# Kernel tuning notes

Hardware: AMD Instinct MI355X
Metric: run time of the kernel (lower is better)

## Reference

```python
import jax, jax.numpy as jnp
import numpy as np

B, T, V, E, H, D = 32, 64, 32000, 512, 1024, 1024
BOS, EOS, PAD, TAU = 1, 3, 0, 1.0


def setup_inputs() -> dict:
    key = jax.random.key(0)
    ks = jax.random.split(key, 8)
    s = lambda k, shape, sc=0.02: jax.random.normal(k, shape, jnp.float32) * sc
    return {
        'image_hidden': jax.random.normal(ks[0], (B, D), jnp.float32),
        'gumbel_u': jax.random.uniform(ks[1], (T, B, V), jnp.float32),
        'W_proj': s(ks[2], (H, D)), 'b_proj': jnp.zeros((H,), jnp.float32),
        'emb': s(ks[3], (V, E)),
        'W_ih': s(ks[4], (4 * H, E)), 'W_hh': s(ks[5], (4 * H, H)),
        'b_ih': jnp.zeros((4 * H,), jnp.float32), 'b_hh': jnp.zeros((4 * H,), jnp.float32),
        'W_hv': s(ks[6], (V, H)), 'b_hv': jnp.zeros((V,), jnp.float32),
    }


def lstm_cell(x, h, c, W_ih, W_hh, b_ih, b_hh):
    gates = x @ W_ih.T + h @ W_hh.T + (b_ih + b_hh)
    i, f, g, o = jnp.split(gates, 4, axis=-1)  # torch LSTM gate order
    c = jax.nn.sigmoid(f) * c + jax.nn.sigmoid(i) * jnp.tanh(g)
    h = jax.nn.sigmoid(o) * jnp.tanh(c)
    return h, c


def reference(image_hidden, gumbel_u, W_proj, b_proj, emb, W_ih, W_hh, b_ih, b_hh, W_hv, b_hv):
    # initial state from projected image representation
    h0 = image_hidden @ W_proj.T + b_proj            # [B, H]
    c0 = jnp.zeros_like(h0)
    x0 = jnp.broadcast_to(emb[BOS], (B, E))          # BOS embedding
    h, c = lstm_cell(x0, h0, c0, W_ih, W_hh, b_ih, b_hh)

    def step(carry, u):
        h, c = carry
        logit = h @ W_hv.T + b_hv                    # [B, V]
        g = -jnp.log(-jnp.log(u + 1e-10) + 1e-10)    # gumbel noise from uniform
        y_soft = jax.nn.softmax((logit + g) / TAU, axis=-1)
        label = jnp.argmax(y_soft, axis=-1)          # [B]
        y_hard = jax.nn.one_hot(label, V, dtype=y_soft.dtype)
        y = y_hard + y_soft - jax.lax.stop_gradient(y_soft)  # straight-through (hard=True)
        x = y @ emb                                  # soft embedding lookup [B, E]
        h, c = lstm_cell(x, h, c, W_ih, W_hh, b_ih, b_hh)
        return (h, c), (y, label)

    _, (ys, labels) = jax.lax.scan(step, (h, c), gumbel_u)
    logits = jnp.swapaxes(ys, 0, 1)                  # [B, T, V]
    labels = labels.T                                # [B, T]

    # force final token to EOS
    logits = logits.at[:, -1, :].set(jax.nn.one_hot(EOS, V, dtype=logits.dtype))
    labels = labels.at[:, -1].set(EOS)

    pad_g = jnp.cumsum((labels == EOS).astype(jnp.int32), axis=1) == 0  # True before first EOS
    message_ids = jnp.where(pad_g, labels, 0)
    pad_oh = jax.nn.one_hot(PAD, V, dtype=logits.dtype)
    message_logits = jnp.where(pad_g[:, :, None], logits, pad_oh)
    message_lengths = jnp.max(jnp.cumsum(pad_g.astype(jnp.int32), axis=1), axis=1) + 1
    return message_ids, message_logits, message_lengths
```

## Files before the change

kernel.cpp:

```cpp
#include <hip/hip_runtime.h>
#include <cstdint>
#include <cstddef>

#define NB 32
#define NT 64
#define NV 32000
#define NE 512
#define NH 1024
#define BOS_ID 1
#define EOS_ID 3
#define KC 64

__device__ __forceinline__ unsigned mono_f32(float f) {
    unsigned u = __float_as_uint(f);
    return (u & 0x80000000u) ? ~u : (u | 0x80000000u);
}

__global__ __launch_bounds__(256) void k_init(const float* __restrict__ img,
                                              const float* __restrict__ Wp,
                                              const float* __restrict__ bp,
                                              float* __restrict__ h0,
                                              float* __restrict__ c) {
    int g = blockIdx.x * 256 + threadIdx.x;
    int j = g >> 5, b = g & 31;
    const float* ir = img + (size_t)b * NH;
    const float* wr = Wp + (size_t)j * NH;
    float s = bp[j];
    for (int k = 0; k < NH; k++) s = fmaf(ir[k], wr[k], s);
    h0[b * NH + j] = s;
    c[b * NH + j]  = 0.0f;
}

__global__ __launch_bounds__(512) void k_logit(const float* __restrict__ h,
                                               const float* __restrict__ Whv,
                                               const float* __restrict__ bhv,
                                               const float* __restrict__ gu,
                                               int s,
                                               unsigned long long* __restrict__ slot) {
    __shared__ float wsh[2][KC][132];
    __shared__ float hs[2][KC][34];
    const int tid = threadIdx.x;
    const int v0  = blockIdx.x * 128;
    const int vq  = tid & 31;
    const int bq  = tid >> 5;
    const int wq  = tid & 15;
    const int wv  = tid >> 4;

    float4 wr[4];
    float4 hr;
    float acc[2][4];
#pragma unroll
    for (int bi = 0; bi < 2; bi++)
#pragma unroll
        for (int j = 0; j < 4; j++) acc[bi][j] = 0.f;

    auto load_chunk = [&](int kc) {
#pragma unroll
        for (int i = 0; i < 4; i++) {
            int vv = i * 32 + wv;
            wr[i] = *(const float4*)&Whv[(size_t)(v0 + vv) * NH + kc + wq * 4];
        }
        hr = *(const float4*)&h[wv * NH + kc + wq * 4];
    };
    auto store_chunk = [&](int p) {
#pragma unroll
        for (int i = 0; i < 4; i++) {
            int vv = i * 32 + wv;
            wsh[p][wq * 4 + 0][vv] = wr[i].x;
            wsh[p][wq * 4 + 1][vv] = wr[i].y;
            wsh[p][wq * 4 + 2][vv] = wr[i].z;
            wsh[p][wq * 4 + 3][vv] = wr[i].w;
        }
        hs[p][wq * 4 + 0][wv] = hr.x;
        hs[p][wq * 4 + 1][wv] = hr.y;
        hs[p][wq * 4 + 2][wv] = hr.z;
        hs[p][wq * 4 + 3][wv] = hr.w;
    };

    load_chunk(0);
    store_chunk(0);
    load_chunk(KC);

    const int NCH = NH / KC;
    for (int c = 0; c < NCH; c++) {
        __syncthreads();
        const int p = c & 1;
#pragma unroll 16
        for (int kk = 0; kk < KC; kk++) {
            float4 wv4 = *(const float4*)&wsh[p][kk][vq * 4];
            float2 hv2 = *(const float2*)&hs[p][kk][bq * 2];
            acc[0][0] = fmaf(hv2.x, wv4.x, acc[0][0]);
            acc[0][1] = fmaf(hv2.x, wv4.y, acc[0][1]);
            acc[0][2] = fmaf(hv2.x, wv4.z, acc[0][2]);
            acc[0][3] = fmaf(hv2.x, wv4.w, acc[0][3]);
            acc[1][0] = fmaf(hv2.y, wv4.x, acc[1][0]);
            acc[1][1] = fmaf(hv2.y, wv4.y, acc[1][1]);
            acc[1][2] = fmaf(hv2.y, wv4.z, acc[1][2]);
            acc[1][3] = fmaf(hv2.y, wv4.w, acc[1][3]);
        }
        if (c + 1 < NCH) {
            store_chunk(1 - p);
            if (c + 2 < NCH) load_chunk((c + 2) * KC);
        }
    }

    const float4 bv4 = *(const float4*)&bhv[v0 + vq * 4];
    float bvv[4] = {bv4.x, bv4.y, bv4.z, bv4.w};
    unsigned long long key[2];
#pragma unroll
    for (int bi = 0; bi < 2; bi++) {
        int b = bq * 2 + bi;
        const float4 u4 = *(const float4*)&gu[((size_t)s * NB + b) * NV + v0 + vq * 4];
        float uvv[4] = {u4.x, u4.y, u4.z, u4.w};
        float best = -3.4e38f;
        int bidx = v0 + vq * 4;
#pragma unroll
        for (int j = 0; j < 4; j++) {
            float g  = -logf(-logf(uvv[j] + 1e-10f) + 1e-10f);
            float sc = acc[bi][j] + bvv[j] + g;
            if (sc > best) { best = sc; bidx = v0 + vq * 4 + j; }
        }
        key[bi] = ((unsigned long long)mono_f32(best) << 32) | (unsigned)(~(unsigned)bidx);
    }
#pragma unroll
    for (int m = 1; m < 32; m <<= 1) {
#pragma unroll
        for (int bi = 0; bi < 2; bi++) {
            unsigned long long o =
                (unsigned long long)__shfl_xor((long long)key[bi], m, 32);
            if (o > key[bi]) key[bi] = o;
        }
    }
    if (vq == 0) {
#pragma unroll
        for (int bi = 0; bi < 2; bi++)
            atomicMax(&slot[(s & 1) * 32 + bq * 2 + bi], key[bi]);
    }
}

__global__ __launch_bounds__(256) void k_lstm(const float* __restrict__ h,
                                              float* __restrict__ hn,
                                              float* __restrict__ cbuf,
                                              const float* __restrict__ emb,
                                              const float* __restrict__ Wih,
                                              const float* __restrict__ Whh,
                                              const float* __restrict__ bih,
                                              const float* __restrict__ bhh,
                                              unsigned long long* __restrict__ slot,
                                              int* __restrict__ hist,
                                              int s, int skip) {
    __shared__ float Wt[512][20];
    __shared__ float xh[32][517];
    __shared__ int labels[32];
    const int tid = threadIdx.x, blk = blockIdx.x;
    const int b8 = tid >> 3, ks = tid & 7;

    if (s < 0) {
        if (tid < 32) labels[tid] = BOS_ID;
    } else {
        if (tid < 32) labels[tid] = (int)(~(unsigned)slot[(s & 1) * 32 + tid]);
    }
    if (tid >= 32 && tid < 64)
        slot[((s + 1) & 1) * 32 + (tid - 32)] = 0ull;
    if (s >= 0 && blk == 0 && tid < 32) hist[s * 32 + tid] = labels[tid];
    if (skip) return;

    const int j0 = blk * 4;
    float acc[16];
#pragma unroll
    for (int r = 0; r < 16; r++) acc[r] = 0.f;

    for (int chunk = 0; chunk < 3; chunk++) {
        __syncthreads();
#pragma unroll
        for (int i = 0; i < 32; i++) {
            int idx = i * 256 + tid;
            int slot_i = idx >> 9, k = idx & 511;
            int gate = slot_i >> 2, jj = slot_i & 3;
            int row = gate * NH + j0 + jj;
            float w = (chunk == 0) ? Wih[(size_t)row * NE + k]
                                   : Whh[(size_t)row * NH + (chunk - 1) * 512 + k];
            Wt[k][slot_i] = w;
        }
#pragma unroll
        for (int i = 0; i < 64; i++) {
            int idx = i * 256 + tid;
            int b = idx >> 9, k = idx & 511;
            float xv = (chunk == 0) ? emb[(size_t)labels[b] * NE + k]
                                    : h[b * NH + (chunk - 1) * 512 + k];
            xh[b][k] = xv;
        }
        __syncthreads();
#pragma unroll 4
        for (int i = 0; i < 64; i++) {
            int k = ks + 8 * i;
            float xv = xh[b8][k];
            const float4 w0 = *(const float4*)&Wt[k][0];
            const float4 w1 = *(const float4*)&Wt[k][4];
            const float4 w2 = *(const float4*)&Wt[k][8];
            const float4 w3 = *(const float4*)&Wt[k][12];
            acc[0]  = fmaf(xv, w0.x, acc[0]);  acc[1]  = fmaf(xv, w0.y, acc[1]);
            acc[2]  = fmaf(xv, w0.z, acc[2]);  acc[3]  = fmaf(xv, w0.w, acc[3]);
            acc[4]  = fmaf(xv, w1.x, acc[4]);  acc[5]  = fmaf(xv, w1.y, acc[5]);
            acc[6]  = fmaf(xv, w1.z, acc[6]);  acc[7]  = fmaf(xv, w1.w, acc[7]);
            acc[8]  = fmaf(xv, w2.x, acc[8]);  acc[9]  = fmaf(xv, w2.y, acc[9]);
            acc[10] = fmaf(xv, w2.z, acc[10]); acc[11] = fmaf(xv, w2.w, acc[11]);
            acc[12] = fmaf(xv, w3.x, acc[12]); acc[13] = fmaf(xv, w3.y, acc[13]);
            acc[14] = fmaf(xv, w3.z, acc[14]); acc[15] = fmaf(xv, w3.w, acc[15]);
        }
    }
#pragma unroll
    for (int m = 1; m < 8; m <<= 1)
#pragma unroll
        for (int r = 0; r < 16; r++) acc[r] += __shfl_xor(acc[r], m, 64);

    if (ks == 0) {
        int b = b8;
#pragma unroll
        for (int jj = 0; jj < 4; jj++) {
            int j = j0 + jj;
            float gi = acc[0 + jj]  + bih[j]          + bhh[j];
            float gf = acc[4 + jj]  + bih[NH + j]     + bhh[NH + j];
            float gg = acc[8 + jj]  + bih[2 * NH + j] + bhh[2 * NH + j];
            float go = acc[12 + jj] + bih[3 * NH + j] + bhh[3 * NH + j];
            float si = 1.f / (1.f + expf(-gi));
            float sf = 1.f / (1.f + expf(-gf));
            float so = 1.f / (1.f + expf(-go));
            float cn = sf * cbuf[b * NH + j] + si * tanhf(gg);
            float hv = so * tanhf(cn);
            cbuf[b * NH + j] = cn;
            hn[b * NH + j]   = hv;
        }
    }
}

__global__ __launch_bounds__(64) void k_out(const int* __restrict__ hist,
                                            float* __restrict__ out) {
    int b = threadIdx.x;
    if (b >= 32) return;
    int te = 63;
    for (int t = 0; t < 63; t++)
        if (hist[t * 32 + b] == EOS_ID) { te = t; break; }
    for (int t = 0; t < 64; t++) {
        int lab = (t < 63) ? hist[t * 32 + b] : EOS_ID;
        int id = (t < te) ? lab : 0;
        out[b * 64 + t] = (float)id;
    }
    out[2048 + (size_t)NB * NT * NV + b] = (float)(te + 1);
}

__global__ __launch_bounds__(256) void k_scatter(float* __restrict__ out) {
    const int bt = blockIdx.x;
    float* row = out + 2048 + (size_t)bt * NV;
    const int id = (int)out[bt];
    float4 z = make_float4(0.f, 0.f, 0.f, 0.f);
    for (int i = threadIdx.x; i < NV / 4; i += 256) ((float4*)row)[i] = z;
    __syncthreads();
    if (threadIdx.x == 0) row[id] = 1.0f;
}

extern "C" void kernel_launch(void* const* d_in, const int* in_sizes, int n_in,
                              void* d_out, int out_size, void* d_ws, size_t ws_size,
                              hipStream_t stream) {
    const float* img = (const float*)d_in[0];
    const float* gu  = (const float*)d_in[1];
    const float* Wp  = (const float*)d_in[2];
    const float* bp  = (const float*)d_in[3];
    const float* emb = (const float*)d_in[4];
    const float* Wih = (const float*)d_in[5];
    const float* Whh = (const float*)d_in[6];
    const float* bih = (const float*)d_in[7];
    const float* bhh = (const float*)d_in[8];
    const float* Whv = (const float*)d_in[9];
    const float* bhv = (const float*)d_in[10];
    float* out = (float*)d_out;

    float* scratch = out + 2048;
    float* hA = scratch;
    float* hB = scratch + 32768;
    float* cb = scratch + 65536;
    unsigned long long* slot = (unsigned long long*)(scratch + 98304);
    int* hist = (int*)(scratch + 98304 + 128);

    k_init<<<128, 256, 0, stream>>>(img, Wp, bp, hB, cb);
    k_lstm<<<256, 256, 0, stream>>>(hB, hA, cb, emb, Wih, Whh, bih, bhh,
                                    slot, hist, -1, 0);
    for (int s = 0; s < 63; s++) {
        const float* hc = (s & 1) ? hB : hA;
        float* hn       = (s & 1) ? hA : hB;
        k_logit<<<250, 512, 0, stream>>>(hc, Whv, bhv, gu, s, slot);
        k_lstm<<<256, 256, 0, stream>>>(hc, hn, cb, emb, Wih, Whh, bih, bhh,
                                        slot, hist, s, (s == 62) ? 1 : 0);
    }
    k_out<<<1, 64, 0, stream>>>(hist, out);
    k_scatter<<<2048, 256, 0, stream>>>(out);
}
```

Baseline: 12.44 ms.

## Retile vocab logit kernel to 64-wide blocks with split-K and swizzled LDS

The logit kernel now covers 64 vocab columns per block instead of 128, doubling the grid to 500 blocks to fill more CUs. Each thread computes a 4x4 batch-by-vocab tile over a quarter of each K chunk, and partial sums are combined with cross-lane shuffles before the Gumbel argmax. Shared-memory tiles use an XOR swizzle so the wider float4 reads avoid bank conflicts. This adds shuffle-reduction work and more atomics per step in exchange for better occupancy and more register-level reuse.

```diff
diff --git a/kernel.cpp b/kernel.cpp
--- a/kernel.cpp
+++ b/kernel.cpp
@@ -10,6 +10,7 @@
 #define BOS_ID 1
 #define EOS_ID 3
 #define KC 64
+#define VB 64
 
 __device__ __forceinline__ unsigned mono_f32(float f) {
     unsigned u = __float_as_uint(f);
@@ -31,32 +32,37 @@
     c[b * NH + j]  = 0.0f;
 }
 
-__global__ __launch_bounds__(512) void k_logit(const float* __restrict__ h,
-                                               const float* __restrict__ Whv,
-                                               const float* __restrict__ bhv,
-                                               const float* __restrict__ gu,
-                                               int s,
-                                               unsigned long long* __restrict__ slot) {
-    __shared__ float wsh[2][KC][132];
-    __shared__ float hs[2][KC][34];
-    const int tid = threadIdx.x;
-    const int v0  = blockIdx.x * 128;
-    const int vq  = tid & 31;
-    const int bq  = tid >> 5;
+__global__ __launch_bounds__(512, 4) void k_logit(const float* __restrict__ h,
+                                                  const float* __restrict__ Whv,
+                                                  const float* __restrict__ bhv,
+                                                  const float* __restrict__ gu,
+                                                  int s,
+                                                  unsigned long long* __restrict__ slot) {
+    __shared__ __align__(16) float wsh[2][KC][68];
+    __shared__ __align__(16) float hs[2][KC][36];
+    const int tid  = threadIdx.x;
+    const int v0   = blockIdx.x * VB;
+    const int lane = tid & 63;
+    const int wb   = tid >> 6;
+    const int kq   = lane >> 4;
+    const int sv   = lane & 15;
+
     const int wq  = tid & 15;
     const int wv  = tid >> 4;
-
-    float4 wr[4];
+    const int mst = (wq & 7) << 2;
+    const int kqs = ((wq >> 2) & 1) << 4;
+
+    float4 wr[2];
     float4 hr;
-    float acc[2][4];
-#pragma unroll
-    for (int bi = 0; bi < 2; bi++)
+    float acc[4][4];
+#pragma unroll
+    for (int bi = 0; bi < 4; bi++)
 #pragma unroll
         for (int j = 0; j < 4; j++) acc[bi][j] = 0.f;
 
     auto load_chunk = [&](int kc) {
 #pragma unroll
-        for (int i = 0; i < 4; i++) {
+        for (int i = 0; i < 2; i++) {
             int vv = i * 32 + wv;
             wr[i] = *(const float4*)&Whv[(size_t)(v0 + vv) * NH + kc + wq * 4];
         }
@@ -64,17 +70,18 @@
     };
     auto store_chunk = [&](int p) {
 #pragma unroll
-        for (int i = 0; i < 4; i++) {
-            int vv = i * 32 + wv;
-            wsh[p][wq * 4 + 0][vv] = wr[i].x;
-            wsh[p][wq * 4 + 1][vv] = wr[i].y;
-            wsh[p][wq * 4 + 2][vv] = wr[i].z;
-            wsh[p][wq * 4 + 3][vv] = wr[i].w;
-        }
-        hs[p][wq * 4 + 0][wv] = hr.x;
-        hs[p][wq * 4 + 1][wv] = hr.y;
-        hs[p][wq * 4 + 2][wv] = hr.z;
-        hs[p][wq * 4 + 3][wv] = hr.w;
+        for (int i = 0; i < 2; i++) {
+            int cb = (i * 32 + wv) ^ mst;
+            wsh[p][wq * 4 + 0][cb] = wr[i].x;
+            wsh[p][wq * 4 + 1][cb] = wr[i].y;
+            wsh[p][wq * 4 + 2][cb] = wr[i].z;
+            wsh[p][wq * 4 + 3][cb] = wr[i].w;
+        }
+        int ch = (wv ^ mst) ^ kqs;
+        hs[p][wq * 4 + 0][ch] = hr.x;
+        hs[p][wq * 4 + 1][ch] = hr.y;
+        hs[p][wq * 4 + 2][ch] = hr.z;
+        hs[p][wq * 4 + 3][ch] = hr.w;
     };
 
     load_chunk(0);
@@ -82,60 +89,73 @@
     load_chunk(KC);
 
     const int NCH = NH / KC;
-    for (int c = 0; c < NCH; c++) {
+    for (int cc = 0; cc < NCH; cc++) {
         __syncthreads();
-        const int p = c & 1;
-#pragma unroll 16
-        for (int kk = 0; kk < KC; kk++) {
-            float4 wv4 = *(const float4*)&wsh[p][kk][vq * 4];
-            float2 hv2 = *(const float2*)&hs[p][kk][bq * 2];
-            acc[0][0] = fmaf(hv2.x, wv4.x, acc[0][0]);
-            acc[0][1] = fmaf(hv2.x, wv4.y, acc[0][1]);
-            acc[0][2] = fmaf(hv2.x, wv4.z, acc[0][2]);
-            acc[0][3] = fmaf(hv2.x, wv4.w, acc[0][3]);
-            acc[1][0] = fmaf(hv2.y, wv4.x, acc[1][0]);
-            acc[1][1] = fmaf(hv2.y, wv4.y, acc[1][1]);
-            acc[1][2] = fmaf(hv2.y, wv4.z, acc[1][2]);
-            acc[1][3] = fmaf(hv2.y, wv4.w, acc[1][3]);
-        }
-        if (c + 1 < NCH) {
+        const int p = cc & 1;
+#pragma unroll
+        for (int i = 0; i < 16; i++) {
+            const int kk = kq * 16 + i;
+            const int m4 = (((kq << 2) + (i >> 2)) & 7) << 2;
+            const float4 w4 = *(const float4*)&wsh[p][kk][(sv << 2) ^ m4];
+            const float4 h4 = *(const float4*)&hs[p][kk][((wb << 2) ^ m4) ^ ((kq & 1) << 4)];
+            acc[0][0] = fmaf(h4.x, w4.x, acc[0][0]);
+            acc[0][1] = fmaf(h4.x, w4.y, acc[0][1]);
+            acc[0][2] = fmaf(h4.x, w4.z, acc[0][2]);
+            acc[0][3] = fmaf(h4.x, w4.w, acc[0][3]);
+            acc[1][0] = fmaf(h4.y, w4.x, acc[1][0]);
+            acc[1][1] = fmaf(h4.y, w4.y, acc[1][1]);
+            acc[1][2] = fmaf(h4.y, w4.z, acc[1][2]);
+            acc[1][3] = fmaf(h4.y, w4.w, acc[1][3]);
+            acc[2][0] = fmaf(h4.z, w4.x, acc[2][0]);
+            acc[2][1] = fmaf(h4.z, w4.y, acc[2][1]);
+            acc[2][2] = fmaf(h4.z, w4.z, acc[2][2]);
+            acc[2][3] = fmaf(h4.z, w4.w, acc[2][3]);
+            acc[3][0] = fmaf(h4.w, w4.x, acc[3][0]);
+            acc[3][1] = fmaf(h4.w, w4.y, acc[3][1]);
+            acc[3][2] = fmaf(h4.w, w4.z, acc[3][2]);
+            acc[3][3] = fmaf(h4.w, w4.w, acc[3][3]);
+        }
+        if (cc + 1 < NCH) {
             store_chunk(1 - p);
-            if (c + 2 < NCH) load_chunk((c + 2) * KC);
-        }
-    }
-
-    const float4 bv4 = *(const float4*)&bhv[v0 + vq * 4];
-    float bvv[4] = {bv4.x, bv4.y, bv4.z, bv4.w};
-    unsigned long long key[2];
-#pragma unroll
-    for (int bi = 0; bi < 2; bi++) {
-        int b = bq * 2 + bi;
-        const float4 u4 = *(const float4*)&gu[((size_t)s * NB + b) * NV + v0 + vq * 4];
-        float uvv[4] = {u4.x, u4.y, u4.z, u4.w};
-        float best = -3.4e38f;
-        int bidx = v0 + vq * 4;
-#pragma unroll
-        for (int j = 0; j < 4; j++) {
-            float g  = -logf(-logf(uvv[j] + 1e-10f) + 1e-10f);
-            float sc = acc[bi][j] + bvv[j] + g;
-            if (sc > best) { best = sc; bidx = v0 + vq * 4 + j; }
-        }
-        key[bi] = ((unsigned long long)mono_f32(best) << 32) | (unsigned)(~(unsigned)bidx);
-    }
-#pragma unroll
-    for (int m = 1; m < 32; m <<= 1) {
-#pragma unroll
-        for (int bi = 0; bi < 2; bi++) {
-            unsigned long long o =
-                (unsigned long long)__shfl_xor((long long)key[bi], m, 32);
-            if (o > key[bi]) key[bi] = o;
-        }
-    }
-    if (vq == 0) {
-#pragma unroll
-        for (int bi = 0; bi < 2; bi++)
-            atomicMax(&slot[(s & 1) * 32 + bq * 2 + bi], key[bi]);
-    }
+            if (cc + 2 < NCH) load_chunk((cc + 2) * KC);
+        }
+    }
+
+    float* af = &acc[0][0];
+#pragma unroll
+    for (int r = 0; r < 16; r++) {
+        af[r] += __shfl_xor(af[r], 16, 64);
+        af[r] += __shfl_xor(af[r], 32, 64);
+    }
+
+    const int b = (wb << 2) + kq;
+    float accsel[4];
+#pragma unroll
+    for (int j = 0; j < 4; j++)
+        accsel[j] = (kq == 0) ? acc[0][j] : (kq == 1) ? acc[1][j]
+                   : (kq == 2) ? acc[2][j] : acc[3][j];
+
+    const float4 bv4 = *(const float4*)&bhv[v0 + (sv << 2)];
+    const float bvv[4] = {bv4.x, bv4.y, bv4.z, bv4.w};
+    const float4 u4 = *(const float4*)&gu[((size_t)s * NB + b) * NV + v0 + (sv << 2)];
+    const float uvv[4] = {u4.x, u4.y, u4.z, u4.w};
+    float best = -3.4e38f;
+    int bidx = v0 + (sv << 2);
+#pragma unroll
+    for (int j = 0; j < 4; j++) {
+        float g  = -logf(-logf(uvv[j] + 1e-10f) + 1e-10f);
+        float sc = accsel[j] + bvv[j] + g;
+        if (sc > best) { best = sc; bidx = v0 + (sv << 2) + j; }
+    }
+    unsigned long long key =
+        ((unsigned long long)mono_f32(best) << 32) | (unsigned)(~(unsigned)bidx);
+#pragma unroll
+    for (int m = 1; m < 16; m <<= 1) {
+        unsigned long long o =
+            (unsigned long long)__shfl_xor((long long)key, m, 64);
+        if (o > key) key = o;
+    }
+    if (sv == 0) atomicMax(&slot[(s & 1) * 32 + b], key);
 }
 
 __global__ __launch_bounds__(256) void k_lstm(const float* __restrict__ h,
@@ -288,7 +308,7 @@
     for (int s = 0; s < 63; s++) {
         const float* hc = (s & 1) ? hB : hA;
         float* hn       = (s & 1) ? hA : hB;
-        k_logit<<<250, 512, 0, stream>>>(hc, Whv, bhv, gu, s, slot);
+        k_logit<<<500, 512, 0, stream>>>(hc, Whv, bhv, gu, s, slot);
         k_lstm<<<256, 256, 0, stream>>>(hc, hn, cb, emb, Wih, Whh, bih, bhh,
                                         slot, hist, s, (s == 62) ? 1 : 0);
     }
```

After: 24.32 ms. +95.4%, slower.

## Rewrite logit GEMV as split-K register kernel and prefetch LSTM chunks into registers

Applied to the files above, without the earlier changes.

The logit kernel drops the LDS double-buffered tiling. Each thread now owns one vocab row and a quarter of K, accumulates all 32 batch rows in registers reading h directly from global/cache, and combines the four K-slices through shared memory before a wave64 argmax reduction. The LSTM kernel issues the next chunk's weight and input loads into registers before computing the current chunk, so global latency overlaps with the FMAs. The costs are much higher register pressure (32 accumulators plus 96 prefetch registers) and heavy redundant reads of h across threads, which may lower occupancy.

```diff
diff --git a/kernel.cpp b/kernel.cpp
--- a/kernel.cpp
+++ b/kernel.cpp
@@ -9,7 +9,6 @@
 #define NH 1024
 #define BOS_ID 1
 #define EOS_ID 3
-#define KC 64
 
 __device__ __forceinline__ unsigned mono_f32(float f) {
     unsigned u = __float_as_uint(f);
@@ -31,110 +30,71 @@
     c[b * NH + j]  = 0.0f;
 }
 
-__global__ __launch_bounds__(512) void k_logit(const float* __restrict__ h,
+__global__ __launch_bounds__(256) void k_logit(const float* __restrict__ h,
                                                const float* __restrict__ Whv,
                                                const float* __restrict__ bhv,
                                                const float* __restrict__ gu,
                                                int s,
                                                unsigned long long* __restrict__ slot) {
-    __shared__ float wsh[2][KC][132];
-    __shared__ float hs[2][KC][34];
+    __shared__ float red[4][64][33];
     const int tid = threadIdx.x;
-    const int v0  = blockIdx.x * 128;
-    const int vq  = tid & 31;
-    const int bq  = tid >> 5;
-    const int wq  = tid & 15;
-    const int wv  = tid >> 4;
-
-    float4 wr[4];
-    float4 hr;
-    float acc[2][4];
-#pragma unroll
-    for (int bi = 0; bi < 2; bi++)
-#pragma unroll
-        for (int j = 0; j < 4; j++) acc[bi][j] = 0.f;
-
-    auto load_chunk = [&](int kc) {
-#pragma unroll
-        for (int i = 0; i < 4; i++) {
-            int vv = i * 32 + wv;
-            wr[i] = *(const float4*)&Whv[(size_t)(v0 + vv) * NH + kc + wq * 4];
-        }
-        hr = *(const float4*)&h[wv * NH + kc + wq * 4];
-    };
-    auto store_chunk = [&](int p) {
-#pragma unroll
-        for (int i = 0; i < 4; i++) {
-            int vv = i * 32 + wv;
-            wsh[p][wq * 4 + 0][vv] = wr[i].x;
-            wsh[p][wq * 4 + 1][vv] = wr[i].y;
-            wsh[p][wq * 4 + 2][vv] = wr[i].z;
-            wsh[p][wq * 4 + 3][vv] = wr[i].w;
-        }
-        hs[p][wq * 4 + 0][wv] = hr.x;
-        hs[p][wq * 4 + 1][wv] = hr.y;
-        hs[p][wq * 4 + 2][wv] = hr.z;
-        hs[p][wq * 4 + 3][wv] = hr.w;
-    };
-
-    load_chunk(0);
-    store_chunk(0);
-    load_chunk(KC);
-
-    const int NCH = NH / KC;
-    for (int c = 0; c < NCH; c++) {
-        __syncthreads();
-        const int p = c & 1;
-#pragma unroll 16
-        for (int kk = 0; kk < KC; kk++) {
-            float4 wv4 = *(const float4*)&wsh[p][kk][vq * 4];
-            float2 hv2 = *(const float2*)&hs[p][kk][bq * 2];
-            acc[0][0] = fmaf(hv2.x, wv4.x, acc[0][0]);
-            acc[0][1] = fmaf(hv2.x, wv4.y, acc[0][1]);
-            acc[0][2] = fmaf(hv2.x, wv4.z, acc[0][2]);
-            acc[0][3] = fmaf(hv2.x, wv4.w, acc[0][3]);
-            acc[1][0] = fmaf(hv2.y, wv4.x, acc[1][0]);
-            acc[1][1] = fmaf(hv2.y, wv4.y, acc[1][1]);
-            acc[1][2] = fmaf(hv2.y, wv4.z, acc[1][2]);
-            acc[1][3] = fmaf(hv2.y, wv4.w, acc[1][3]);
-        }
-        if (c + 1 < NCH) {
-            store_chunk(1 - p);
-            if (c + 2 < NCH) load_chunk((c + 2) * KC);
-        }
-    }
-
-    const float4 bv4 = *(const float4*)&bhv[v0 + vq * 4];
-    float bvv[4] = {bv4.x, bv4.y, bv4.z, bv4.w};
-    unsigned long long key[2];
-#pragma unroll
-    for (int bi = 0; bi < 2; bi++) {
-        int b = bq * 2 + bi;
-        const float4 u4 = *(const float4*)&gu[((size_t)s * NB + b) * NV + v0 + vq * 4];
-        float uvv[4] = {u4.x, u4.y, u4.z, u4.w};
-        float best = -3.4e38f;
-        int bidx = v0 + vq * 4;
-#pragma unroll
-        for (int j = 0; j < 4; j++) {
-            float g  = -logf(-logf(uvv[j] + 1e-10f) + 1e-10f);
-            float sc = acc[bi][j] + bvv[j] + g;
-            if (sc > best) { best = sc; bidx = v0 + vq * 4 + j; }
-        }
-        key[bi] = ((unsigned long long)mono_f32(best) << 32) | (unsigned)(~(unsigned)bidx);
-    }
-#pragma unroll
-    for (int m = 1; m < 32; m <<= 1) {
-#pragma unroll
-        for (int bi = 0; bi < 2; bi++) {
+    const int w   = tid >> 6;
+    const int l   = tid & 63;
+    const int v   = blockIdx.x * 64 + l;
+    const float* __restrict__ wrow = Whv + (size_t)v * NH + w * 256;
+    const float* __restrict__ hq   = h + w * 256;
+
+    float acc[32];
+#pragma unroll
+    for (int b = 0; b < 32; b++) acc[b] = 0.f;
+
+    for (int c = 0; c < 16; c++) {
+        const float4 w0 = *(const float4*)&wrow[c * 16 + 0];
+        const float4 w1 = *(const float4*)&wrow[c * 16 + 4];
+        const float4 w2 = *(const float4*)&wrow[c * 16 + 8];
+        const float4 w3 = *(const float4*)&wrow[c * 16 + 12];
+#pragma unroll
+        for (int b = 0; b < 32; b++) {
+            const float* hb = &hq[b * NH + c * 16];
+            const float4 h0 = *(const float4*)&hb[0];
+            const float4 h1 = *(const float4*)&hb[4];
+            const float4 h2 = *(const float4*)&hb[8];
+            const float4 h3 = *(const float4*)&hb[12];
+            float a = acc[b];
+            a = fmaf(h0.x, w0.x, a); a = fmaf(h0.y, w0.y, a);
+            a = fmaf(h0.z, w0.z, a); a = fmaf(h0.w, w0.w, a);
+            a = fmaf(h1.x, w1.x, a); a = fmaf(h1.y, w1.y, a);
+            a = fmaf(h1.z, w1.z, a); a = fmaf(h1.w, w1.w, a);
+            a = fmaf(h2.x, w2.x, a); a = fmaf(h2.y, w2.y, a);
+            a = fmaf(h2.z, w2.z, a); a = fmaf(h2.w, w2.w, a);
+            a = fmaf(h3.x, w3.x, a); a = fmaf(h3.y, w3.y, a);
+            a = fmaf(h3.z, w3.z, a); a = fmaf(h3.w, w3.w, a);
+            acc[b] = a;
+        }
+    }
+
+#pragma unroll
+    for (int b = 0; b < 32; b++) red[w][l][b] = acc[b];
+    __syncthreads();
+
+    const float bv = bhv[v];
+    const size_t gubase = (size_t)s * NB * NV;
+#pragma unroll
+    for (int i = 0; i < 8; i++) {
+        const int b = w * 8 + i;
+        float f = ((red[0][l][b] + red[1][l][b]) + red[2][l][b]) + red[3][l][b];
+        float u = gu[gubase + (size_t)b * NV + v];
+        float g  = -logf(-logf(u + 1e-10f) + 1e-10f);
+        float sc = f + bv + g;
+        unsigned long long key =
+            ((unsigned long long)mono_f32(sc) << 32) | (unsigned)(~(unsigned)v);
+#pragma unroll
+        for (int m = 1; m < 64; m <<= 1) {
             unsigned long long o =
-                (unsigned long long)__shfl_xor((long long)key[bi], m, 32);
-            if (o > key[bi]) key[bi] = o;
-        }
-    }
-    if (vq == 0) {
-#pragma unroll
-        for (int bi = 0; bi < 2; bi++)
-            atomicMax(&slot[(s & 1) * 32 + bq * 2 + bi], key[bi]);
+                (unsigned long long)__shfl_xor((long long)key, m, 64);
+            if (o > key) key = o;
+        }
+        if (l == 0) atomicMax(&slot[(s & 1) * 32 + b], key);
     }
 }
 
@@ -170,26 +130,42 @@
 #pragma unroll
     for (int r = 0; r < 16; r++) acc[r] = 0.f;
 
-    for (int chunk = 0; chunk < 3; chunk++) {
-        __syncthreads();
+    float wreg[32];
+    float xreg[64];
+    auto issue = [&](int chunk) {
 #pragma unroll
         for (int i = 0; i < 32; i++) {
             int idx = i * 256 + tid;
             int slot_i = idx >> 9, k = idx & 511;
             int gate = slot_i >> 2, jj = slot_i & 3;
             int row = gate * NH + j0 + jj;
-            float w = (chunk == 0) ? Wih[(size_t)row * NE + k]
+            wreg[i] = (chunk == 0) ? Wih[(size_t)row * NE + k]
                                    : Whh[(size_t)row * NH + (chunk - 1) * 512 + k];
-            Wt[k][slot_i] = w;
         }
 #pragma unroll
         for (int i = 0; i < 64; i++) {
             int idx = i * 256 + tid;
             int b = idx >> 9, k = idx & 511;
-            float xv = (chunk == 0) ? emb[(size_t)labels[b] * NE + k]
-                                    : h[b * NH + (chunk - 1) * 512 + k];
-            xh[b][k] = xv;
-        }
+            xreg[i] = (chunk == 0) ? emb[(size_t)labels[b] * NE + k]
+                                   : h[b * NH + (chunk - 1) * 512 + k];
+        }
+    };
+
+    __syncthreads();
+    issue(0);
+    for (int chunk = 0; chunk < 3; chunk++) {
+        __syncthreads();
+#pragma unroll
+        for (int i = 0; i < 32; i++) {
+            int idx = i * 256 + tid;
+            Wt[idx & 511][idx >> 9] = wreg[i];
+        }
+#pragma unroll
+        for (int i = 0; i < 64; i++) {
+            int idx = i * 256 + tid;
+            xh[idx >> 9][idx & 511] = xreg[i];
+        }
+        if (chunk < 2) issue(chunk + 1);
         __syncthreads();
 #pragma unroll 4
         for (int i = 0; i < 64; i++) {
@@ -288,7 +264,7 @@
     for (int s = 0; s < 63; s++) {
         const float* hc = (s & 1) ? hB : hA;
         float* hn       = (s & 1) ? hA : hB;
-        k_logit<<<250, 512, 0, stream>>>(hc, Whv, bhv, gu, s, slot);
+        k_logit<<<500, 256, 0, stream>>>(hc, Whv, bhv, gu, s, slot);
         k_lstm<<<256, 256, 0, stream>>>(hc, hn, cb, emb, Wih, Whh, bih, bhh,
                                         slot, hist, s, (s == 62) ? 1 : 0);
     }
```

Measured after the change: 15.88 ms. 27.6% more time.
